# Kernel tuning notes

Measured on AMD Instinct MI355X. Metric: run time of the kernel, lower is better.

## Reference

```python
import jax, jax.numpy as jnp
from jax import lax
import numpy as np

B, T, D_IN = 1024, 64, 1662
H1, H2, H3 = 64, 128, 64


def _lstm_layer(x, w_ih, w_hh, b_ih, b_hh):
    """PyTorch-convention single-layer LSTM. x: [B,T,D]; gate order i,f,g,o."""
    Bc = x.shape[0]
    H = w_hh.shape[1]
    # Precompute input contribution for all timesteps: [B,T,4H]
    xg = jnp.einsum('btd,gd->btg', x, w_ih) + b_ih + b_hh

    def step(carry, xt):
        h, c = carry
        gates = xt + h @ w_hh.T  # [B,4H]
        i, f, g, o = jnp.split(gates, 4, axis=-1)
        i = jax.nn.sigmoid(i)
        f = jax.nn.sigmoid(f)
        g = jnp.tanh(g)
        o = jax.nn.sigmoid(o)
        c = f * c + i * g
        h = o * jnp.tanh(c)
        return (h, c), h

    h0 = jnp.zeros((Bc, H), x.dtype)
    (_, _), hs = lax.scan(step, (h0, h0), jnp.swapaxes(xg, 0, 1))
    return jnp.swapaxes(hs, 0, 1)  # [B,T,H]


def setup_inputs() -> dict:
    key = jax.random.key(0)
    ks = jax.random.split(key, 20)

    def u(k, shape, fan):
        bound = 1.0 / np.sqrt(fan)
        return jax.random.uniform(k, shape, jnp.float32, -bound, bound)

    x = jax.random.normal(ks[0], (B, T, D_IN), jnp.float32)
    return {
        'x': x,
        'w_ih1': u(ks[1], (4 * H1, D_IN), H1), 'w_hh1': u(ks[2], (4 * H1, H1), H1),
        'b_ih1': u(ks[3], (4 * H1,), H1),      'b_hh1': u(ks[4], (4 * H1,), H1),
        'w_ih2': u(ks[5], (4 * H2, H1), H2),   'w_hh2': u(ks[6], (4 * H2, H2), H2),
        'b_ih2': u(ks[7], (4 * H2,), H2),      'b_hh2': u(ks[8], (4 * H2,), H2),
        'w_ih3': u(ks[9], (4 * H3, H2), H3),   'w_hh3': u(ks[10], (4 * H3, H3), H3),
        'b_ih3': u(ks[11], (4 * H3,), H3),     'b_hh3': u(ks[12], (4 * H3,), H3),
        'fc1_w': u(ks[13], (64, 64), 64),      'fc1_b': u(ks[14], (64,), 64),
        'fc2_w': u(ks[15], (32, 64), 64),      'fc2_b': u(ks[16], (32,), 64),
        'fc3_w': u(ks[17], (3, 32), 32),       'fc3_b': u(ks[18], (3,), 32),
    }


def reference(x, w_ih1, w_hh1, b_ih1, b_hh1,
              w_ih2, w_hh2, b_ih2, b_hh2,
              w_ih3, w_hh3, b_ih3, b_hh3,
              fc1_w, fc1_b, fc2_w, fc2_b, fc3_w, fc3_b):
    h = _lstm_layer(x, w_ih1, w_hh1, b_ih1, b_hh1)   # [B,T,64]
    h = _lstm_layer(h, w_ih2, w_hh2, b_ih2, b_hh2)   # [B,T,128]
    h = _lstm_layer(h, w_ih3, w_hh3, b_ih3, b_hh3)   # [B,T,64]
    h = h[:, -1, :]                                   # [B,64]
    h = jax.nn.relu(h @ fc1_w.T + fc1_b)
    h = jax.nn.relu(h @ fc2_w.T + fc2_b)
    return jax.nn.softmax(h @ fc3_w.T + fc3_b, axis=1)  # [B,3]
```

## Files before the change

kernel.cpp:

```cpp
#include <hip/hip_runtime.h>
#include <hip/hip_bf16.h>

#define B_SZ   1024
#define T_SZ   64
#define D_IN   1662
#define D_INP  1664
#define M_SZ   (B_SZ * T_SZ)

typedef __attribute__((ext_vector_type(8))) short short8;
typedef __attribute__((ext_vector_type(4))) float f32x4;
typedef unsigned short ushort_t;

__device__ __forceinline__ unsigned short f2bf(float f) {
    unsigned u = __builtin_bit_cast(unsigned, f);
    u += 0x7FFFu + ((u >> 16) & 1u);
    return (unsigned short)(u >> 16);
}
__device__ __forceinline__ float bf2f(ushort_t u) {
    return __builtin_bit_cast(float, (unsigned)u << 16);
}

#define GLD16(gp, lp) __builtin_amdgcn_global_load_lds(                        \
    (const __attribute__((address_space(1))) void*)(gp),                       \
    (__attribute__((address_space(3))) void*)(lp), 16, 0, 0)

__device__ __forceinline__ float sigmoid_f(float x) {
    return 1.0f / (1.0f + __expf(-x));
}
__device__ __forceinline__ float tanh_f(float x) {
    float a = fabsf(x);
    float e = __expf(2.0f * a);
    float r = 1.0f - 2.0f / (e + 1.0f);
    return copysignf(r, x);
}

__global__ __launch_bounds__(256) void convert_w1(
    const float* __restrict__ src, ushort_t* __restrict__ dst)
{
    constexpr int cpr = D_INP >> 3;
    const int total = 256 * cpr;
    const int stride = gridDim.x * blockDim.x;
    for (int idx = blockIdx.x * blockDim.x + threadIdx.x;
         idx < total; idx += stride) {
        const int row  = idx / cpr;
        const int base = (idx % cpr) << 3;
        const float* s = src + (size_t)row * D_IN;
        short8 o;
        #pragma unroll
        for (int j = 0; j < 4; ++j) {
            const int k = base + 2 * j;
            float2 v = make_float2(0.f, 0.f);
            if (k < D_IN) v = *(const float2*)(s + k);
            o[2 * j]     = (short)f2bf(v.x);
            o[2 * j + 1] = (short)f2bf(v.y);
        }
        *(short8*)(dst + (size_t)row * D_INP + base) = o;
    }
}

__global__ __launch_bounds__(512, 2) void gemm_l1(
    const float* __restrict__ A, const ushort_t* __restrict__ W,
    ushort_t* __restrict__ out)
{
    constexpr int K = D_IN, Kp = D_INP, G = 256;
    __shared__ __align__(16) ushort_t As[128 * 32];
    __shared__ __align__(16) ushort_t Ws[256 * 32];

    const int tid = threadIdx.x, lane = tid & 63, wid = tid >> 6;
    const int wr = wid >> 2, wc = wid & 3;
    const int m0 = blockIdx.x * 128;

    const int arow  = tid >> 2;
    const int acolb = (tid & 3) * 8;
    const float* Abase = A + (size_t)(m0 + arow) * K + acolb;

    const size_t wlofs = (size_t)(lane >> 2) * Kp + (lane & 3) * 8;
    const ushort_t* Wg0 = W + (size_t)(wid * 32) * Kp + wlofs;
    const ushort_t* Wg1 = Wg0 + (size_t)16 * Kp;
    ushort_t* lw0 = &Ws[(wid * 32) * 32];
    ushort_t* lw1 = lw0 + 16 * 32;

    const int fr = lane & 15, kq = (lane >> 4) * 8;

    f32x4 acc[4][4] = {};
    const int nFull = K / 32;

    float2 av[4];
    #pragma unroll
    for (int j = 0; j < 4; ++j) av[j] = *(const float2*)(Abase + 2 * j);

    for (int it = 0; it <= nFull; ++it) {
        const int k0 = it * 32;
        __syncthreads();
        GLD16(Wg0 + k0, lw0); GLD16(Wg1 + k0, lw1);
        short8 pk;
        #pragma unroll
        for (int j = 0; j < 4; ++j) {
            pk[2 * j]     = (short)f2bf(av[j].x);
            pk[2 * j + 1] = (short)f2bf(av[j].y);
        }
        *(short8*)&As[arow * 32 + acolb] = pk;
        __syncthreads();

        if (it < nFull) {
            const int kn = (it + 1) * 32;
            if (it + 1 < nFull) {
                #pragma unroll
                for (int j = 0; j < 4; ++j)
                    av[j] = *(const float2*)(Abase + kn + 2 * j);
            } else {
                #pragma unroll
                for (int j = 0; j < 4; ++j) {
                    const int kk = kn + acolb + 2 * j;
                    av[j] = (kk < K) ? *(const float2*)(Abase + kn + 2 * j)
                                     : make_float2(0.f, 0.f);
                }
            }
        }

        short8 af[4], bfr[4];
        #pragma unroll
        for (int fm = 0; fm < 4; ++fm)
            af[fm] = *(const short8*)&As[(wr * 64 + fm * 16 + fr) * 32 + kq];
        #pragma unroll
        for (int fn = 0; fn < 4; ++fn)
            bfr[fn] = *(const short8*)&Ws[(wc * 64 + fn * 16 + fr) * 32 + kq];
        #pragma unroll
        for (int fm = 0; fm < 4; ++fm)
            #pragma unroll
            for (int fn = 0; fn < 4; ++fn)
                acc[fm][fn] = __builtin_amdgcn_mfma_f32_16x16x32_bf16(
                    af[fm], bfr[fn], acc[fm][fn], 0, 0, 0);
    }

    const int rbase = (lane >> 4) * 4;
    #pragma unroll
    for (int fn = 0; fn < 4; ++fn) {
        const int g = wc * 64 + fn * 16 + fr;
        #pragma unroll
        for (int fm = 0; fm < 4; ++fm) {
            const int mbase = m0 + wr * 64 + fm * 16 + rbase;
            #pragma unroll
            for (int j = 0; j < 4; ++j)
                out[(size_t)(mbase + j) * G + g] = f2bf(acc[fm][fn][j]);
        }
    }
}

__global__ __launch_bounds__(512, 2) void lstm3_gg(
    const ushort_t* __restrict__ xg1,
    const float* __restrict__ whh1,
    const float* __restrict__ bih1, const float* __restrict__ bhh1,
    const float* __restrict__ wih2, const float* __restrict__ whh2,
    const float* __restrict__ bih2, const float* __restrict__ bhh2,
    const float* __restrict__ wih3, const float* __restrict__ whh3,
    const float* __restrict__ bih3, const float* __restrict__ bhh3,
    float* __restrict__ hlast, int Tn)
{
    __shared__ ushort_t h1sh[2][16 * 64];
    __shared__ ushort_t h2sh[2][16 * 128];
    __shared__ ushort_t h3sh[2][16 * 64];
    __shared__ __align__(16) ushort_t xsh[2][1024];
    __shared__ __align__(16) float gsw[8][128 * 4];

    const int tid = threadIdx.x, lane = tid & 63, wid = tid >> 6;
    const int r0 = blockIdx.x * 4;
    const int fr = lane & 15, hi = lane >> 4, kq = hi * 8;

    int role, ubase, Hl;
    if (wid < 2)      { role = 1; ubase = wid * 32;       Hl = 64; }
    else if (wid < 6) { role = 2; ubase = (wid - 2) * 32; Hl = 128; }
    else              { role = 3; ubase = (wid - 6) * 32; Hl = 64; }

    short8 bregS[2][4][2];
    short8 bregL[2][4][4];
    #pragma unroll
    for (int ut = 0; ut < 2; ++ut)
        #pragma unroll
        for (int g = 0; g < 4; ++g) {
            const int uu = ubase + ut * 16 + fr;
            const float *pS, *pL = nullptr;
            if (role == 1)      { pS = whh1 + (size_t)(g * 64 + uu) * 64; }
            else if (role == 2) { pS = wih2 + (size_t)(g * 128 + uu) * 64;
                                  pL = whh2 + (size_t)(g * 128 + uu) * 128; }
            else                { pS = whh3 + (size_t)(g * 64 + uu) * 64;
                                  pL = wih3 + (size_t)(g * 64 + uu) * 128; }
            #pragma unroll
            for (int ks = 0; ks < 2; ++ks) {
                const float4 v0 = *(const float4*)(pS + ks * 32 + kq);
                const float4 v1 = *(const float4*)(pS + ks * 32 + kq + 4);
                short8 b;
                b[0] = (short)f2bf(v0.x); b[1] = (short)f2bf(v0.y);
                b[2] = (short)f2bf(v0.z); b[3] = (short)f2bf(v0.w);
                b[4] = (short)f2bf(v1.x); b[5] = (short)f2bf(v1.y);
                b[6] = (short)f2bf(v1.z); b[7] = (short)f2bf(v1.w);
                bregS[ut][g][ks] = b;
            }
            if (role >= 2) {
                #pragma unroll
                for (int ks = 0; ks < 4; ++ks) {
                    const float4 v0 = *(const float4*)(pL + ks * 32 + kq);
                    const float4 v1 = *(const float4*)(pL + ks * 32 + kq + 4);
                    short8 b;
                    b[0] = (short)f2bf(v0.x); b[1] = (short)f2bf(v0.y);
                    b[2] = (short)f2bf(v0.z); b[3] = (short)f2bf(v0.w);
                    b[4] = (short)f2bf(v1.x); b[5] = (short)f2bf(v1.y);
                    b[6] = (short)f2bf(v1.z); b[7] = (short)f2bf(v1.w);
                    bregL[ut][g][ks] = b;
                }
            }
        }

    float bias[2][4];
    {
        const float* bihp = (role == 1) ? bih1 : (role == 2) ? bih2 : bih3;
        const float* bhhp = (role == 1) ? bhh1 : (role == 2) ? bhh2 : bhh3;
        #pragma unroll
        for (int i = 0; i < 2; ++i) {
            const int unit = ubase + i * 16 + fr;
            #pragma unroll
            for (int g = 0; g < 4; ++g)
                bias[i][g] = bihp[g * Hl + unit] + bhhp[g * Hl + unit];
        }
    }

    for (int i = tid; i < 16 * 64; i += 512) {
        h1sh[0][i] = 0; h1sh[1][i] = 0;
        h3sh[0][i] = 0; h3sh[1][i] = 0;
    }
    for (int i = tid; i < 16 * 128; i += 512) { h2sh[0][i] = 0; h2sh[1][i] = 0; }

    if (tid < 128) {
        const int rw = tid >> 5, xc = (tid & 31) * 8;
        *(short8*)&xsh[0][rw * 256 + xc] =
            *(const short8*)(xg1 + ((size_t)(r0 + rw) * Tn) * 256 + xc);
    }

    float c[2] = {0.f, 0.f};
    __syncthreads();

    const int nSteps = Tn + 2;
    for (int s = 0; s < nSteps; ++s) {
        const int rb = s & 1, wb = rb ^ 1;

        if (wid < 2 && s + 1 < Tn) {
            const int rw = wid * 2 + (lane >> 5);
            const int xc = (lane & 31) * 8;
            GLD16(xg1 + ((size_t)(r0 + rw) * Tn + (s + 1)) * 256 + xc,
                  &xsh[wb][wid * 512]);
        }

        const bool act = (role == 1) ? (s < Tn)
                       : (role == 2) ? (s >= 1 && s <= Tn)
                                     : (s >= 2 && s <= Tn + 1);
        if (act) {
            short8 aS[2], aL[4];
            const ushort_t* srcS = (role == 3) ? h3sh[rb] : h1sh[rb];
            #pragma unroll
            for (int ks = 0; ks < 2; ++ks) {
                const int k0 = ks * 32 + kq;
                aS[ks] = *(const short8*)&srcS[fr * 64 + (k0 ^ ((fr & 7) << 3))];
            }
            if (role >= 2) {
                #pragma unroll
                for (int ks = 0; ks < 4; ++ks) {
                    const int k0 = ks * 32 + kq;
                    aL[ks] = *(const short8*)
                        &h2sh[rb][fr * 128 + (k0 ^ ((fr & 7) << 3))];
                }
            }

            #pragma unroll
            for (int ut = 0; ut < 2; ++ut)
                #pragma unroll
                for (int g = 0; g < 4; ++g) {
                    f32x4 acc = {};
                    #pragma unroll
                    for (int ks = 0; ks < 2; ++ks)
                        acc = __builtin_amdgcn_mfma_f32_16x16x32_bf16(
                            aS[ks], bregS[ut][g][ks], acc, 0, 0, 0);
                    if (role >= 2) {
                        #pragma unroll
                        for (int ks = 0; ks < 4; ++ks)
                            acc = __builtin_amdgcn_mfma_f32_16x16x32_bf16(
                                aL[ks], bregL[ut][g][ks], acc, 0, 0, 0);
                    }
                    if (hi == 0)
                        *(f32x4*)&gsw[wid][(g * 32 + ut * 16 + fr) * 4] = acc;
                }

            #pragma unroll
            for (int i = 0; i < 2; ++i) {
                const int uloc = i * 16 + fr;
                const int unit = ubase + uloc;
                float gi = gsw[wid][(0 * 32 + uloc) * 4 + hi] + bias[i][0];
                float gf = gsw[wid][(1 * 32 + uloc) * 4 + hi] + bias[i][1];
                float gg = gsw[wid][(2 * 32 + uloc) * 4 + hi] + bias[i][2];
                float go = gsw[wid][(3 * 32 + uloc) * 4 + hi] + bias[i][3];
                if (role == 1) {
                    const ushort_t* xb = &xsh[rb][hi * 256 + unit];
                    gi += bf2f(xb[0]);   gf += bf2f(xb[64]);
                    gg += bf2f(xb[128]); go += bf2f(xb[192]);
                }
                const float iv = sigmoid_f(gi);
                const float fv = sigmoid_f(gf);
                const float gv = tanh_f(gg);
                const float ov = sigmoid_f(go);
                c[i] = fmaf(fv, c[i], iv * gv);
                const float h = ov * tanh_f(c[i]);
                ushort_t* hdst = (role == 1) ? h1sh[wb]
                               : (role == 2) ? h2sh[wb] : h3sh[wb];
                hdst[hi * Hl + (unit ^ (hi << 3))] = f2bf(h);
                if (role == 3 && s == Tn + 1)
                    hlast[(size_t)(r0 + hi) * 64 + unit] = h;
            }
        }
        __syncthreads();
    }
}

__global__ __launch_bounds__(256) void head_kernel(
    const float* __restrict__ hlast,
    const float* __restrict__ w1, const float* __restrict__ b1,
    const float* __restrict__ w2, const float* __restrict__ b2,
    const float* __restrict__ w3, const float* __restrict__ b3,
    float* __restrict__ out)
{
    __shared__ float W1[64][64];
    __shared__ float W2[32][64];
    __shared__ float W3[3][32];
    __shared__ float hin[16][64];
    __shared__ float a1[16][64];
    __shared__ float a2[16][32];
    __shared__ float lg[16][3];

    const int tid = threadIdx.x;
    const int r0 = blockIdx.x * 16;

    for (int i = tid; i < 64 * 64; i += 256) W1[i >> 6][i & 63] = w1[i];
    for (int i = tid; i < 32 * 64; i += 256) W2[i >> 6][i & 63] = w2[i];
    for (int i = tid; i < 3 * 32; i += 256) W3[i >> 5][i & 31] = w3[i];
    for (int i = tid; i < 16 * 64; i += 256) {
        int r = i >> 6, u = i & 63;
        hin[r][u] = hlast[(size_t)(r0 + r) * 64 + u];
    }
    __syncthreads();

    for (int i = tid; i < 16 * 64; i += 256) {
        int r = i >> 6, j = i & 63;
        float s = b1[j];
        #pragma unroll
        for (int k = 0; k < 64; ++k) s = fmaf(hin[r][k], W1[j][k], s);
        a1[r][j] = fmaxf(s, 0.f);
    }
    __syncthreads();

    for (int i = tid; i < 16 * 32; i += 256) {
        int r = i >> 5, j = i & 31;
        float s = b2[j];
        #pragma unroll
        for (int k = 0; k < 64; ++k) s = fmaf(a1[r][k], W2[j][k], s);
        a2[r][j] = fmaxf(s, 0.f);
    }
    __syncthreads();

    for (int i = tid; i < 16 * 3; i += 256) {
        int r = i / 3, j = i % 3;
        float s = b3[j];
        #pragma unroll
        for (int k = 0; k < 32; ++k) s = fmaf(a2[r][k], W3[j][k], s);
        lg[r][j] = s;
    }
    __syncthreads();

    if (tid < 16) {
        float l0 = lg[tid][0], l1 = lg[tid][1], l2 = lg[tid][2];
        float m = fmaxf(l0, fmaxf(l1, l2));
        float e0 = __expf(l0 - m), e1 = __expf(l1 - m), e2 = __expf(l2 - m);
        float inv = 1.0f / (e0 + e1 + e2);
        out[(size_t)(r0 + tid) * 3 + 0] = e0 * inv;
        out[(size_t)(r0 + tid) * 3 + 1] = e1 * inv;
        out[(size_t)(r0 + tid) * 3 + 2] = e2 * inv;
    }
}

extern "C" void kernel_launch(void* const* d_in, const int* in_sizes, int n_in,
                              void* d_out, int out_size, void* d_ws, size_t ws_size,
                              hipStream_t stream)
{
    const float* x    = (const float*)d_in[0];
    const float* wih1 = (const float*)d_in[1];
    const float* whh1 = (const float*)d_in[2];
    const float* bih1 = (const float*)d_in[3];
    const float* bhh1 = (const float*)d_in[4];
    const float* wih2 = (const float*)d_in[5];
    const float* whh2 = (const float*)d_in[6];
    const float* bih2 = (const float*)d_in[7];
    const float* bhh2 = (const float*)d_in[8];
    const float* wih3 = (const float*)d_in[9];
    const float* whh3 = (const float*)d_in[10];
    const float* bih3 = (const float*)d_in[11];
    const float* bhh3 = (const float*)d_in[12];
    const float* f1w  = (const float*)d_in[13];
    const float* f1b  = (const float*)d_in[14];
    const float* f2w  = (const float*)d_in[15];
    const float* f2b  = (const float*)d_in[16];
    const float* f3w  = (const float*)d_in[17];
    const float* f3b  = (const float*)d_in[18];
    float* outp = (float*)d_out;

    char* wsb = (char*)d_ws;
    size_t off = 0;
    ushort_t* bufA  = (ushort_t*)(wsb + off); off += 33554432;
    float*    hlast = (float*)(wsb + off);    off += 262144;
    ushort_t* w1b   = (ushort_t*)(wsb + off);

    const int T = T_SZ;

    convert_w1<<<208, 256, 0, stream>>>(wih1, w1b);

    gemm_l1<<<M_SZ / 128, 512, 0, stream>>>(x, w1b, bufA);

    lstm3_gg<<<B_SZ / 4, 512, 0, stream>>>(
        bufA, whh1, bih1, bhh1,
        wih2, whh2, bih2, bhh2,
        wih3, whh3, bih3, bhh3,
        hlast, T);

    head_kernel<<<B_SZ / 16, 256, 0, stream>>>(
        hlast, f1w, f1b, f2w, f2b, f3w, f3b, outp);
}
```

Measured before the change: 336.9 us.

## Halve batch rows per LSTM block to double block count and occupancy

The fused three-layer LSTM kernel now handles 2 batch rows per block instead of 4, and the grid grows from 256 to 512 blocks. Each lane now computes one (unit, row) cell per step instead of two, so the per-step elementwise work, bias registers and cell state per thread are halved. The x-gate prefetch needs only one wave. The goal is to put two blocks on each CU so the serial recurrence steps of different blocks can overlap and hide latency. The cost is that the 16-row MFMA tiles are now even more padded, so total matrix instructions double.

```diff
diff --git a/kernel.cpp b/kernel.cpp
--- a/kernel.cpp
+++ b/kernel.cpp
@@ -160,11 +160,11 @@
     __shared__ ushort_t h1sh[2][16 * 64];
     __shared__ ushort_t h2sh[2][16 * 128];
     __shared__ ushort_t h3sh[2][16 * 64];
-    __shared__ __align__(16) ushort_t xsh[2][1024];
+    __shared__ __align__(16) ushort_t xsh[2][512];
     __shared__ __align__(16) float gsw[8][128 * 4];
 
     const int tid = threadIdx.x, lane = tid & 63, wid = tid >> 6;
-    const int r0 = blockIdx.x * 4;
+    const int r0 = blockIdx.x * 2;
     const int fr = lane & 15, hi = lane >> 4, kq = hi * 8;
 
     int role, ubase, Hl;
@@ -211,17 +211,17 @@
             }
         }
 
-    float bias[2][4];
+    const int itile = hi >> 1;
+    const int row   = hi & 1;
+    const int uloc  = itile * 16 + fr;
+    const int unit  = ubase + uloc;
+    float bias[4];
     {
         const float* bihp = (role == 1) ? bih1 : (role == 2) ? bih2 : bih3;
         const float* bhhp = (role == 1) ? bhh1 : (role == 2) ? bhh2 : bhh3;
         #pragma unroll
-        for (int i = 0; i < 2; ++i) {
-            const int unit = ubase + i * 16 + fr;
-            #pragma unroll
-            for (int g = 0; g < 4; ++g)
-                bias[i][g] = bihp[g * Hl + unit] + bhhp[g * Hl + unit];
-        }
+        for (int g = 0; g < 4; ++g)
+            bias[g] = bihp[g * Hl + unit] + bhhp[g * Hl + unit];
     }
 
     for (int i = tid; i < 16 * 64; i += 512) {
@@ -230,24 +230,23 @@
     }
     for (int i = tid; i < 16 * 128; i += 512) { h2sh[0][i] = 0; h2sh[1][i] = 0; }
 
-    if (tid < 128) {
+    if (tid < 64) {
         const int rw = tid >> 5, xc = (tid & 31) * 8;
         *(short8*)&xsh[0][rw * 256 + xc] =
             *(const short8*)(xg1 + ((size_t)(r0 + rw) * Tn) * 256 + xc);
     }
 
-    float c[2] = {0.f, 0.f};
+    float c = 0.f;
     __syncthreads();
 
     const int nSteps = Tn + 2;
     for (int s = 0; s < nSteps; ++s) {
         const int rb = s & 1, wb = rb ^ 1;
 
-        if (wid < 2 && s + 1 < Tn) {
-            const int rw = wid * 2 + (lane >> 5);
-            const int xc = (lane & 31) * 8;
-            GLD16(xg1 + ((size_t)(r0 + rw) * Tn + (s + 1)) * 256 + xc,
-                  &xsh[wb][wid * 512]);
+        if (wid == 0 && s + 1 < Tn) {
+            GLD16(xg1 + ((size_t)(r0 + (lane >> 5)) * Tn + (s + 1)) * 256
+                      + (lane & 31) * 8,
+                  &xsh[wb][0]);
         }
 
         const bool act = (role == 1) ? (s < Tn)
@@ -289,16 +288,13 @@
                         *(f32x4*)&gsw[wid][(g * 32 + ut * 16 + fr) * 4] = acc;
                 }
 
-            #pragma unroll
-            for (int i = 0; i < 2; ++i) {
-                const int uloc = i * 16 + fr;
-                const int unit = ubase + uloc;
-                float gi = gsw[wid][(0 * 32 + uloc) * 4 + hi] + bias[i][0];
-                float gf = gsw[wid][(1 * 32 + uloc) * 4 + hi] + bias[i][1];
-                float gg = gsw[wid][(2 * 32 + uloc) * 4 + hi] + bias[i][2];
-                float go = gsw[wid][(3 * 32 + uloc) * 4 + hi] + bias[i][3];
+            {
+                float gi = gsw[wid][(0 * 32 + uloc) * 4 + row] + bias[0];
+                float gf = gsw[wid][(1 * 32 + uloc) * 4 + row] + bias[1];
+                float gg = gsw[wid][(2 * 32 + uloc) * 4 + row] + bias[2];
+                float go = gsw[wid][(3 * 32 + uloc) * 4 + row] + bias[3];
                 if (role == 1) {
-                    const ushort_t* xb = &xsh[rb][hi * 256 + unit];
+                    const ushort_t* xb = &xsh[rb][row * 256 + unit];
                     gi += bf2f(xb[0]);   gf += bf2f(xb[64]);
                     gg += bf2f(xb[128]); go += bf2f(xb[192]);
                 }
@@ -306,13 +302,13 @@
                 const float fv = sigmoid_f(gf);
                 const float gv = tanh_f(gg);
                 const float ov = sigmoid_f(go);
-                c[i] = fmaf(fv, c[i], iv * gv);
-                const float h = ov * tanh_f(c[i]);
+                c = fmaf(fv, c, iv * gv);
+                const float h = ov * tanh_f(c);
                 ushort_t* hdst = (role == 1) ? h1sh[wb]
                                : (role == 2) ? h2sh[wb] : h3sh[wb];
-                hdst[hi * Hl + (unit ^ (hi << 3))] = f2bf(h);
+                hdst[row * Hl + (unit ^ (row << 3))] = f2bf(h);
                 if (role == 3 && s == Tn + 1)
-                    hlast[(size_t)(r0 + hi) * 64 + unit] = h;
+                    hlast[(size_t)(r0 + row) * 64 + unit] = h;
             }
         }
         __syncthreads();
@@ -421,7 +417,7 @@
 
     gemm_l1<<<M_SZ / 128, 512, 0, stream>>>(x, w1b, bufA);
 
-    lstm3_gg<<<B_SZ / 4, 512, 0, stream>>>(
+    lstm3_gg<<<B_SZ / 2, 512, 0, stream>>>(
         bufA, whh1, bih1, bhh1,
         wih2, whh2, bih2, bhh2,
         wih3, whh3, bih3, bhh3,
```

Result: slower. 449.4 us (+33.4%).
